# Kernel optimization log

Hardware: AMD Instinct MI355X
Metric: run time of the kernel (lower is better)

## Reference

```python
import jax, jax.numpy as jnp
import numpy as np

H, DH = 16, 64  # n_head, head_dim


def setup_inputs() -> dict:
    key = jax.random.key(0)
    ks = jax.random.split(key, 14)
    B, L, D = 2, 1024, 1024
    d = DH

    def lin_w(k, fan_in, shape):
        return jax.random.normal(k, shape, jnp.float32) / np.sqrt(fan_in)

    return {
        "x": jax.random.normal(ks[0], (B, L, D), jnp.float32),
        "Wq": lin_w(ks[1], D, (D, D)),
        "bq": jnp.zeros((D,), jnp.float32),
        "Wk1": lin_w(ks[2], D, (D, D)),
        "bk1": jnp.zeros((D,), jnp.float32),
        "Wk2": lin_w(ks[3], D, (D, D)),
        "bk2": jnp.zeros((D,), jnp.float32),
        "Wg": lin_w(ks[4], d, (d, 1)),
        "bg": jnp.zeros((1,), jnp.float32),
        "Ws": lin_w(ks[5], d, (d, 1)),
        "bs": jnp.zeros((1,), jnp.float32),
        "Wp": lin_w(ks[6], D, (D, D)),
        "bp": jnp.zeros((D,), jnp.float32),
    }


def reference(x, Wq, bq, Wk1, bk1, Wk2, bk2, Wg, bg, Ws, bs, Wp, bp):
    B, L, D = x.shape
    d = DH
    # AR (GLA) branch
    Q = (x @ Wq + bq).reshape(B, L, H, d)
    K = (x @ Wk1 + bk1).reshape(B, L, H, d)
    V = x.reshape(B, L, H, d)
    W = jnp.einsum('blhd,blhe->blhde', K, V)  # (B,L,H,d,d) outer products
    # stable cumprod of sigmoid gate via log-cumsum-exp trick
    G = jax.nn.sigmoid(x.reshape(B, L, H, d) @ Wg + bg)            # (B,L,H,1)
    log_cum = jnp.clip(jnp.cumsum(jnp.log(jnp.clip(G, 1e-6, None)), axis=1), -30.0, 30.0)
    Gc = (jnp.exp(log_cum) + 1e-6)[..., None]                       # (B,L,H,1,1)
    R = jax.nn.silu(K @ Ws + bs)[..., None]                         # (B,L,H,1,1) decay gate
    Wc = jnp.cumsum(W * R / Gc, axis=1) * Gc                        # weighted cumsum
    O1 = jnp.einsum('blhd,blhde->blhe', Q, Wc)                      # (B,L,H,d)
    # MA branch on one-step residuals
    E = V[:, 1:] - O1[:, :-1]                                       # (B,L-1,H,d)
    q2 = -jax.nn.leaky_relu(-Q[:, :-1] / np.sqrt(d), 0.02)          # ma_q_activation (scale head_dim)
    k2 = jax.nn.sigmoid((x[:, :-1] @ Wk2 + bk2) / np.sqrt(D) * 0.02)  # ma_k_activation (scale n_embd)
    k2 = k2.reshape(B, L - 1, H, d)
    W_ma = jnp.cumsum(jnp.einsum('blhd,blhe->blhde', k2, E), axis=1)
    O2 = jnp.einsum('blhd,blhde->blhe', q2, W_ma)
    O2 = jnp.concatenate([jnp.zeros_like(O2[:, :1]), O2], axis=1)   # shift: first MA output is 0
    O = (O1 + O2).reshape(B, L, D)
    return O @ Wp + bp
```

## Files before the change

kernel.cpp:

```cpp
#include <hip/hip_runtime.h>
#include <hip/hip_bf16.h>
#include <math.h>

#define B_  2
#define L_  1024
#define D_  1024
#define H_  16
#define DH_ 64
#define M_  (B_*L_)
#define CHUNK 64
#define NCH (L_/CHUNK)
#define PT 72
#define PS 68

#define KSCALE (0.02f/32.0f)

using bf16x8 = __attribute__((ext_vector_type(8))) short;
using f32x4  = __attribute__((ext_vector_type(4))) float;

__device__ __forceinline__ unsigned short bf16r(float f){
  union{float f; unsigned int u;} x; x.f = f;
  unsigned int r = x.u + 0x7FFF + ((x.u>>16)&1);
  return (unsigned short)(r>>16);
}
__device__ __forceinline__ float bf2f(unsigned short u){
  union{unsigned int u; float f;} x; x.u = ((unsigned int)u)<<16; return x.f;
}

__device__ __forceinline__ void gate_prefix(
  const float* __restrict__ GL, const float* __restrict__ RR,
  int bh, int c, int l, float* cf_s, float* gc_s)
{
  const float* g = GL + (size_t)bh*L_;
  float part = 0.f;
  for (int i = l; i < c*64; i += 64) part += g[i];
  #pragma unroll
  for (int off = 32; off; off >>= 1) part += __shfl_xor(part, off);
  float x = g[c*64 + l];
  #pragma unroll
  for (int off = 1; off < 64; off <<= 1){
    float t = __shfl_up(x, off);
    if (l >= off) x += t;
  }
  float cum = part + x;
  float lc = fminf(fmaxf(cum, -30.f), 30.f);
  float gc = expf(lc) + 1e-6f;
  cf_s[l] = RR[(size_t)bh*L_ + c*64 + l] / gc;
  if (gc_s) gc_s[l] = gc;
}

__device__ __forceinline__ void chunk_carry(
  const float* __restrict__ csb, int c, int tid, float* carry)
{
  #pragma unroll
  for (int i=0;i<16;i++) carry[i] = 0.f;
  const float4* cb = (const float4*)(csb + (size_t)tid*16);
  #pragma unroll 2
  for (int c2=0;c2<c;c2++){
    const float4* p4 = cb + (size_t)c2*1024;
    float4 a0=p4[0],a1=p4[1],a2=p4[2],a3=p4[3];
    carry[0]+=a0.x; carry[1]+=a0.y; carry[2]+=a0.z; carry[3]+=a0.w;
    carry[4]+=a1.x; carry[5]+=a1.y; carry[6]+=a1.z; carry[7]+=a1.w;
    carry[8]+=a2.x; carry[9]+=a2.y; carry[10]+=a2.z; carry[11]+=a2.w;
    carry[12]+=a3.x; carry[13]+=a3.y; carry[14]+=a3.z; carry[15]+=a3.w;
  }
}

__global__ __launch_bounds__(256) void convert_all(
  const float* __restrict__ X,
  const float* __restrict__ W0, const float* __restrict__ W1,
  const float* __restrict__ W2, const float* __restrict__ W3,
  unsigned short* __restrict__ Xbf,
  unsigned short* __restrict__ T0, unsigned short* __restrict__ T1,
  unsigned short* __restrict__ T2, unsigned short* __restrict__ T3)
{
  int z = blockIdx.z;
  if (z == 4) {
    int row = blockIdx.x*64 + (threadIdx.x>>2);
    int col = blockIdx.y*64 + (threadIdx.x&3)*16;
    const float4* src = (const float4*)&X[(size_t)row*D_ + col];
    float4 a=src[0], b=src[1], c=src[2], d=src[3];
    unsigned short buf[16] = {
      bf16r(a.x),bf16r(a.y),bf16r(a.z),bf16r(a.w),
      bf16r(b.x),bf16r(b.y),bf16r(b.z),bf16r(b.w),
      bf16r(c.x),bf16r(c.y),bf16r(c.z),bf16r(c.w),
      bf16r(d.x),bf16r(d.y),bf16r(d.z),bf16r(d.w)};
    *(uint4*)&Xbf[(size_t)row*D_ + col]     = *(uint4*)&buf[0];
    *(uint4*)&Xbf[(size_t)row*D_ + col + 8] = *(uint4*)&buf[8];
    return;
  }
  if (blockIdx.x >= 16) return;
  const float* W = z==0?W0: z==1?W1: z==2?W2: W3;
  unsigned short* T = z==0?T0: z==1?T1: z==2?T2: T3;
  __shared__ float tile[64][65];
  int kBase = blockIdx.x*64, nBase = blockIdx.y*64;
  #pragma unroll
  for (int i=0;i<16;i++){
    int idx = threadIdx.x + i*256;
    int r = idx>>6, c = idx&63;
    tile[r][c] = W[(size_t)(kBase+r)*D_ + nBase+c];
  }
  __syncthreads();
  #pragma unroll
  for (int i=0;i<16;i++){
    int idx = threadIdx.x + i*256;
    int n = idx>>6, k = idx&63;
    T[(size_t)(nBase+n)*D_ + kBase+k] = bf16r(tile[k][n]);
  }
}

__global__ __launch_bounds__(256) void gemm3(
  const unsigned short* __restrict__ A,
  const unsigned short* __restrict__ T0, const unsigned short* __restrict__ T1,
  const unsigned short* __restrict__ T2,
  const float* __restrict__ b0, const float* __restrict__ b1, const float* __restrict__ b2,
  unsigned short* __restrict__ F0, unsigned short* __restrict__ F1,
  unsigned short* __restrict__ F2)
{
  int z = blockIdx.z;
  const unsigned short* Bt = z==0?T0: z==1?T1: T2;
  const float* bias = z==0?b0: z==1?b1: b2;
  unsigned short* F = z==0?F0: z==1?F1: F2;
  int epi = (z==2) ? 1 : 0;
  int rowBase = blockIdx.x*128, colBase = blockIdx.y*128;

  __shared__ __align__(16) unsigned short As[128*32];
  __shared__ __align__(16) unsigned short Bs[128*32];
  int tid = threadIdx.x, w = tid>>6, l = tid&63;
  int lr = l&15, g4 = l>>4;
  int wr = w>>1, wc = w&1;
  f32x4 acc[4][4];
  #pragma unroll
  for (int mi=0;mi<4;mi++)
    #pragma unroll
    for (int ni=0;ni<4;ni++)
      acc[mi][ni] = (f32x4){0.f,0.f,0.f,0.f};

  for (int k0 = 0; k0 < D_; k0 += 32) {
    #pragma unroll
    for (int i=0;i<2;i++){
      int Fi = (w*2+i)*64 + l;
      int r = Fi>>2, c16 = Fi&3;
      int sc = c16 ^ ((r>>1)&3);
      const unsigned short* ga = A  + (size_t)(rowBase+r)*D_ + k0 + sc*8;
      const unsigned short* gb = Bt + (size_t)(colBase+r)*D_ + k0 + sc*8;
      __builtin_amdgcn_global_load_lds(
        (const __attribute__((address_space(1))) void*)ga,
        (__attribute__((address_space(3))) void*)(As + (size_t)(w*2+i)*512), 16, 0, 0);
      __builtin_amdgcn_global_load_lds(
        (const __attribute__((address_space(1))) void*)gb,
        (__attribute__((address_space(3))) void*)(Bs + (size_t)(w*2+i)*512), 16, 0, 0);
    }
    __syncthreads();
    bf16x8 af[4], bfr[4];
    #pragma unroll
    for (int mi=0;mi<4;mi++){
      int row = wr*64 + mi*16 + lr;
      af[mi] = *(const bf16x8*)(As + row*32 + ((g4 ^ ((row>>1)&3))*8));
    }
    #pragma unroll
    for (int ni=0;ni<4;ni++){
      int n = wc*64 + ni*16 + lr;
      bfr[ni] = *(const bf16x8*)(Bs + n*32 + ((g4 ^ ((n>>1)&3))*8));
    }
    #pragma unroll
    for (int mi=0;mi<4;mi++)
      #pragma unroll
      for (int ni=0;ni<4;ni++)
        acc[mi][ni] = __builtin_amdgcn_mfma_f32_16x16x32_bf16(af[mi], bfr[ni], acc[mi][ni], 0,0,0);
    __syncthreads();
  }

  #pragma unroll
  for (int mi=0;mi<4;mi++){
    #pragma unroll
    for (int ni=0;ni<4;ni++){
      int col = colBase + wc*64 + ni*16 + lr;
      float bv = bias[col];
      #pragma unroll
      for (int r=0;r<4;r++){
        int row = rowBase + wr*64 + mi*16 + g4*4 + r;
        float v = acc[mi][ni][r] + bv;
        if (epi) v = 1.f/(1.f + expf(-v*KSCALE));
        F[(size_t)row*D_ + col] = bf16r(v);
      }
    }
  }
}

__global__ __launch_bounds__(256) void gemm1(
  const unsigned short* __restrict__ A, const unsigned short* __restrict__ Bt,
  const float* __restrict__ bias, float* __restrict__ C)
{
  int rowBase = blockIdx.x*128, colBase = blockIdx.y*64;
  __shared__ __align__(16) unsigned short As[128*32];
  __shared__ __align__(16) unsigned short Bs[64*32];
  int tid = threadIdx.x, w = tid>>6, l = tid&63;
  int lr = l&15, g4 = l>>4;
  f32x4 acc[2][4];
  #pragma unroll
  for (int mi=0;mi<2;mi++)
    #pragma unroll
    for (int ni=0;ni<4;ni++)
      acc[mi][ni] = (f32x4){0.f,0.f,0.f,0.f};

  for (int k0 = 0; k0 < D_; k0 += 32) {
    #pragma unroll
    for (int i=0;i<2;i++){
      int F = (w*2+i)*64 + l;
      int r = F>>2, c16 = F&3;
      int sc = c16 ^ ((r>>1)&3);
      const unsigned short* g = A + (size_t)(rowBase+r)*D_ + k0 + sc*8;
      __builtin_amdgcn_global_load_lds(
        (const __attribute__((address_space(1))) void*)g,
        (__attribute__((address_space(3))) void*)(As + (size_t)(w*2+i)*512), 16, 0, 0);
    }
    {
      int F = w*64 + l;
      int r = F>>2, c16 = F&3;
      int sc = c16 ^ ((r>>1)&3);
      const unsigned short* g = Bt + (size_t)(colBase+r)*D_ + k0 + sc*8;
      __builtin_amdgcn_global_load_lds(
        (const __attribute__((address_space(1))) void*)g,
        (__attribute__((address_space(3))) void*)(Bs + (size_t)w*512), 16, 0, 0);
    }
    __syncthreads();
    bf16x8 af[2], bfr[4];
    #pragma unroll
    for (int mi=0;mi<2;mi++){
      int row = w*32 + mi*16 + lr;
      af[mi] = *(const bf16x8*)(As + row*32 + ((g4 ^ ((row>>1)&3))*8));
    }
    #pragma unroll
    for (int ni=0;ni<4;ni++){
      int n = ni*16 + lr;
      bfr[ni] = *(const bf16x8*)(Bs + n*32 + ((g4 ^ ((n>>1)&3))*8));
    }
    #pragma unroll
    for (int mi=0;mi<2;mi++)
      #pragma unroll
      for (int ni=0;ni<4;ni++)
        acc[mi][ni] = __builtin_amdgcn_mfma_f32_16x16x32_bf16(af[mi], bfr[ni], acc[mi][ni], 0,0,0);
    __syncthreads();
  }

  #pragma unroll
  for (int mi=0;mi<2;mi++){
    #pragma unroll
    for (int ni=0;ni<4;ni++){
      int col = colBase + ni*16 + lr;
      float bv = bias[col];
      #pragma unroll
      for (int r=0;r<4;r++){
        int row = rowBase + w*32 + mi*16 + g4*4 + r;
        C[(size_t)row*D_ + col] = acc[mi][ni][r] + bv;
      }
    }
  }
}

__global__ __launch_bounds__(256) void scalars_kernel(
  const float* __restrict__ X, const unsigned short* __restrict__ Kbf,
  const float* __restrict__ Wg, const float* __restrict__ bg,
  const float* __restrict__ Ws, const float* __restrict__ bs,
  float* __restrict__ GL, float* __restrict__ RR)
{
  int item = blockIdx.x * 4 + (threadIdx.x >> 6);
  int ln = threadIdx.x & 63;
  int row = item >> 4;
  int h = item & 15;
  float xv = X[(size_t)row*D_ + h*64 + ln];
  float kv = bf2f(Kbf[(size_t)row*D_ + h*64 + ln]);
  float gdot = xv * Wg[ln];
  float rdot = kv * Ws[ln];
  #pragma unroll
  for (int off = 32; off; off >>= 1) {
    gdot += __shfl_xor(gdot, off);
    rdot += __shfl_xor(rdot, off);
  }
  if (ln == 0) {
    int b = row >> 10, l = row & 1023;
    size_t o = (size_t)(b*16 + h)*L_ + l;
    float glogit = gdot + bg[0];
    float sg = 1.f/(1.f+expf(-glogit));
    sg = fmaxf(sg, 1e-6f);
    GL[o] = logf(sg);
    float rlogit = rdot + bs[0];
    RR[o] = rlogit / (1.f + expf(-rlogit));
  }
}

__global__ __launch_bounds__(256) void ar_chunk_sum(
  const unsigned short* __restrict__ Kbf, const unsigned short* __restrict__ Xbf,
  const float* __restrict__ GL, const float* __restrict__ RR,
  float* __restrict__ CS)
{
  int bh = blockIdx.x, c = blockIdx.y;
  int b = bh >> 4, h = bh & 15;
  int row0 = b*L_ + c*CHUNK;
  __shared__ __align__(16) unsigned short kt_t[64*PT];
  __shared__ __align__(16) unsigned short cv_t[64*PT];
  __shared__ __align__(16) float uni[64*PS];
  __shared__ float cf_s[64];
  int tid = threadIdx.x;
  if (tid < 64) gate_prefix(GL, RR, bh, c, tid, cf_s, nullptr);
  __syncthreads();
  const unsigned short* kg = Kbf + (size_t)row0*D_ + h*64;
  const unsigned short* vg = Xbf + (size_t)row0*D_ + h*64;
  #pragma unroll
  for (int t=0;t<2;t++){
    int j = (tid>>3) + t*32;
    int d0 = (tid&7)*8;
    bf16x8 kv = *(const bf16x8*)&kg[(size_t)j*D_ + d0];
    bf16x8 vv = *(const bf16x8*)&vg[(size_t)j*D_ + d0];
    float cfj = cf_s[j];
    #pragma unroll
    for (int i=0;i<8;i++){
      kt_t[(d0+i)*PT + j] = (unsigned short)kv[i];
      cv_t[(d0+i)*PT + j] = bf16r(bf2f((unsigned short)vv[i]) * cfj);
    }
  }
  __syncthreads();
  int w = tid>>6, l = tid&63, lr = l&15, g4 = l>>4;
  f32x4 acc[4];
  #pragma unroll
  for (int ni=0;ni<4;ni++) acc[ni] = (f32x4){0.f,0.f,0.f,0.f};
  #pragma unroll
  for (int kk=0;kk<2;kk++){
    bf16x8 a = *(const bf16x8*)&cv_t[(w*16+lr)*PT + kk*32 + g4*8];
    #pragma unroll
    for (int ni=0;ni<4;ni++){
      bf16x8 bb = *(const bf16x8*)&kt_t[(ni*16+lr)*PT + kk*32 + g4*8];
      acc[ni] = __builtin_amdgcn_mfma_f32_16x16x32_bf16(a, bb, acc[ni], 0,0,0);
    }
  }
  #pragma unroll
  for (int ni=0;ni<4;ni++)
    #pragma unroll
    for (int r=0;r<4;r++)
      uni[(w*16+g4*4+r)*PS + ni*16+lr] = acc[ni][r];
  __syncthreads();
  float* out = CS + ((size_t)bh*NCH + c)*4096;
  #pragma unroll
  for (int t=0;t<4;t++){
    int idx = tid + t*256;
    int r = idx>>4, s = idx&15;
    *(float4*)&out[r*64 + s*4] = *(float4*)&uni[r*PS + s*4];
  }
}

__global__ __launch_bounds__(256) void ar_o1_fused(
  const unsigned short* __restrict__ Qbf, const unsigned short* __restrict__ Kbf,
  const unsigned short* __restrict__ Xbf, const unsigned short* __restrict__ K2bf,
  const float* __restrict__ GL, const float* __restrict__ RR,
  const float* __restrict__ CSA, float* __restrict__ CSM,
  float* __restrict__ O1)
{
  int bh = blockIdx.x, c = blockIdx.y;
  int b = bh >> 4, h = bh & 15;
  int row0 = b*L_ + c*CHUNK;
  __shared__ __align__(16) unsigned short q_t[64*PT];
  __shared__ __align__(16) unsigned short k_t[64*PT];
  __shared__ __align__(16) unsigned short vt_t[64*PT];
  __shared__ __align__(16) float uni[64*PS];
  unsigned short* p_t = (unsigned short*)uni;
  __shared__ float cf_s[64], gc_s[64];
  int tid = threadIdx.x;
  if (tid < 64) gate_prefix(GL, RR, bh, c, tid, cf_s, gc_s);
  const unsigned short* qg = Qbf + (size_t)row0*D_ + h*64;
  const unsigned short* kg = Kbf + (size_t)row0*D_ + h*64;
  const unsigned short* vg = Xbf + (size_t)row0*D_ + h*64;
  float carry[16];
  chunk_carry(CSA + (size_t)bh*NCH*4096, c, tid, carry);
  #pragma unroll
  for (int t=0;t<2;t++){
    int idx = tid + t*256;
    int j = idx>>3, s = idx&7;
    *(uint4*)&q_t[j*PT + s*8] = *(const uint4*)&qg[(size_t)j*D_ + s*8];
    *(uint4*)&k_t[j*PT + s*8] = *(const uint4*)&kg[(size_t)j*D_ + s*8];
  }
  #pragma unroll
  for (int t=0;t<2;t++){
    int j = (tid>>3) + t*32;
    int e0 = (tid&7)*8;
    bf16x8 vv = *(const bf16x8*)&vg[(size_t)j*D_ + e0];
    #pragma unroll
    for (int i=0;i<8;i++) vt_t[(e0+i)*PT + j] = (unsigned short)vv[i];
  }
  __syncthreads();
  int w = tid>>6, l = tid&63, lr = l&15, g4 = l>>4;
  f32x4 acc[4];
  #pragma unroll
  for (int ni=0;ni<4;ni++) acc[ni] = (f32x4){0.f,0.f,0.f,0.f};
  #pragma unroll
  for (int kk=0;kk<2;kk++){
    bf16x8 a = *(const bf16x8*)&q_t[(w*16+lr)*PT + kk*32 + g4*8];
    #pragma unroll
    for (int ni=0;ni<4;ni++){
      bf16x8 bb = *(const bf16x8*)&k_t[(ni*16+lr)*PT + kk*32 + g4*8];
      acc[ni] = __builtin_amdgcn_mfma_f32_16x16x32_bf16(a, bb, acc[ni], 0,0,0);
    }
  }
  #pragma unroll
  for (int ni=0;ni<4;ni++){
    int j = ni*16 + lr;
    float cf = cf_s[j];
    #pragma unroll
    for (int r=0;r<4;r++){
      int row = w*16 + g4*4 + r;
      float v = (j <= row) ? acc[ni][r]*cf : 0.f;
      p_t[row*PT + j] = bf16r(v);
    }
  }
  __syncthreads();
  {
    unsigned short buf[16];
    #pragma unroll
    for (int i=0;i<16;i++) buf[i] = bf16r(carry[i]);
    int row = tid>>2, col = (tid&3)*16;
    *(uint4*)&k_t[row*PT + col]     = *(uint4*)&buf[0];
    *(uint4*)&k_t[row*PT + col + 8] = *(uint4*)&buf[8];
  }
  __syncthreads();
  #pragma unroll
  for (int ni=0;ni<4;ni++) acc[ni] = (f32x4){0.f,0.f,0.f,0.f};
  #pragma unroll
  for (int kk=0;kk<2;kk++){
    bf16x8 ap = *(const bf16x8*)&p_t[(w*16+lr)*PT + kk*32 + g4*8];
    bf16x8 aq = *(const bf16x8*)&q_t[(w*16+lr)*PT + kk*32 + g4*8];
    #pragma unroll
    for (int ni=0;ni<4;ni++){
      bf16x8 bv = *(const bf16x8*)&vt_t[(ni*16+lr)*PT + kk*32 + g4*8];
      bf16x8 bs = *(const bf16x8*)&k_t[(ni*16+lr)*PT + kk*32 + g4*8];
      acc[ni] = __builtin_amdgcn_mfma_f32_16x16x32_bf16(ap, bv, acc[ni], 0,0,0);
      acc[ni] = __builtin_amdgcn_mfma_f32_16x16x32_bf16(aq, bs, acc[ni], 0,0,0);
    }
  }
  __syncthreads();
  #pragma unroll
  for (int ni=0;ni<4;ni++)
    #pragma unroll
    for (int r=0;r<4;r++){
      int row = w*16 + g4*4 + r;
      uni[row*PS + ni*16 + lr] = gc_s[row]*acc[ni][r];
    }
  __syncthreads();
  #pragma unroll
  for (int t=0;t<4;t++){
    int idx = tid + t*256;
    int r = idx>>4, s = idx&15;
    *(float4*)&O1[(size_t)(row0+r)*D_ + h*64 + s*4] = *(float4*)&uni[r*PS + s*4];
  }
  #pragma unroll
  for (int t=0;t<2;t++){
    int j = (tid>>3) + t*32;
    int d0 = (tid&7)*8;
    bf16x8 kv = *(const bf16x8*)&K2bf[(size_t)(row0+j)*D_ + h*64 + d0];
    float ev[8] = {0.f,0.f,0.f,0.f,0.f,0.f,0.f,0.f};
    if (c*CHUNK + j < L_-1){
      bf16x8 xv = *(const bf16x8*)&Xbf[(size_t)(row0+j+1)*D_ + h*64 + d0];
      #pragma unroll
      for (int i=0;i<8;i++) ev[i] = bf2f((unsigned short)xv[i]) - uni[j*PS + d0 + i];
    }
    #pragma unroll
    for (int i=0;i<8;i++){
      vt_t[(d0+i)*PT + j] = (unsigned short)kv[i];
      k_t [(d0+i)*PT + j] = bf16r(ev[i]);
    }
  }
  __syncthreads();
  f32x4 acc2[4];
  #pragma unroll
  for (int ni=0;ni<4;ni++) acc2[ni] = (f32x4){0.f,0.f,0.f,0.f};
  #pragma unroll
  for (int kk=0;kk<2;kk++){
    bf16x8 a = *(const bf16x8*)&k_t[(w*16+lr)*PT + kk*32 + g4*8];
    #pragma unroll
    for (int ni=0;ni<4;ni++){
      bf16x8 bb = *(const bf16x8*)&vt_t[(ni*16+lr)*PT + kk*32 + g4*8];
      acc2[ni] = __builtin_amdgcn_mfma_f32_16x16x32_bf16(a, bb, acc2[ni], 0,0,0);
    }
  }
  __syncthreads();
  #pragma unroll
  for (int ni=0;ni<4;ni++)
    #pragma unroll
    for (int r=0;r<4;r++)
      uni[(w*16+g4*4+r)*PS + ni*16+lr] = acc2[ni][r];
  __syncthreads();
  float* outm = CSM + ((size_t)bh*NCH + c)*4096;
  #pragma unroll
  for (int t=0;t<4;t++){
    int idx = tid + t*256;
    int r = idx>>4, s = idx&15;
    *(float4*)&outm[r*64 + s*4] = *(float4*)&uni[r*PS + s*4];
  }
}

__global__ __launch_bounds__(256) void ma_o2_mfma(
  const unsigned short* __restrict__ Qbf, const unsigned short* __restrict__ K2bf,
  const unsigned short* __restrict__ Xbf, const float* __restrict__ CS,
  const float* __restrict__ O1, unsigned short* __restrict__ Obf)
{
  int bh = blockIdx.x, c = blockIdx.y;
  int b = bh >> 4, h = bh & 15;
  int row0 = b*L_ + c*CHUNK;
  __shared__ __align__(16) unsigned short q_t[64*PT];
  __shared__ __align__(16) unsigned short k_t[64*PT];
  __shared__ __align__(16) unsigned short et_t[64*PT];
  __shared__ __align__(16) float uni[64*PS];
  unsigned short* p_t = (unsigned short*)uni;
  int tid = threadIdx.x;
  const unsigned short* qg = Qbf  + (size_t)row0*D_ + h*64;
  const unsigned short* kg = K2bf + (size_t)row0*D_ + h*64;
  float carry[16];
  chunk_carry(CS + (size_t)bh*NCH*4096, c, tid, carry);
  #pragma unroll
  for (int t=0;t<2;t++){
    int idx = tid + t*256;
    int j = idx>>3, s = idx&7;
    *(uint4*)&k_t[j*PT + s*8] = *(const uint4*)&kg[(size_t)j*D_ + s*8];
  }
  #pragma unroll
  for (int t=0;t<2;t++){
    int j = (tid>>3) + t*32;
    int d0 = (tid&7)*8;
    bf16x8 qv = *(const bf16x8*)&qg[(size_t)j*D_ + d0];
    unsigned short qb[8];
    #pragma unroll
    for (int i=0;i<8;i++){
      float q = bf2f((unsigned short)qv[i]);
      qb[i] = bf16r((q > 0.f ? 0.02f*q : q) * 0.125f);
    }
    *(uint4*)&q_t[j*PT + d0] = *(uint4*)&qb[0];
    float ev[8] = {0.f,0.f,0.f,0.f,0.f,0.f,0.f,0.f};
    if (c*CHUNK + j < L_-1){
      bf16x8 xv = *(const bf16x8*)&Xbf[(size_t)(row0+j+1)*D_ + h*64 + d0];
      const float4* op = (const float4*)&O1[(size_t)(row0+j)*D_ + h*64 + d0];
      float4 o0 = op[0], o1v = op[1];
      ev[0]=bf2f((unsigned short)xv[0])-o0.x;  ev[1]=bf2f((unsigned short)xv[1])-o0.y;
      ev[2]=bf2f((unsigned short)xv[2])-o0.z;  ev[3]=bf2f((unsigned short)xv[3])-o0.w;
      ev[4]=bf2f((unsigned short)xv[4])-o1v.x; ev[5]=bf2f((unsigned short)xv[5])-o1v.y;
      ev[6]=bf2f((unsigned short)xv[6])-o1v.z; ev[7]=bf2f((unsigned short)xv[7])-o1v.w;
    }
    #pragma unroll
    for (int i=0;i<8;i++) et_t[(d0+i)*PT + j] = bf16r(ev[i]);
  }
  __syncthreads();
  int w = tid>>6, l = tid&63, lr = l&15, g4 = l>>4;
  f32x4 acc[4];
  #pragma unroll
  for (int ni=0;ni<4;ni++) acc[ni] = (f32x4){0.f,0.f,0.f,0.f};
  #pragma unroll
  for (int kk=0;kk<2;kk++){
    bf16x8 a = *(const bf16x8*)&q_t[(w*16+lr)*PT + kk*32 + g4*8];
    #pragma unroll
    for (int ni=0;ni<4;ni++){
      bf16x8 bb = *(const bf16x8*)&k_t[(ni*16+lr)*PT + kk*32 + g4*8];
      acc[ni] = __builtin_amdgcn_mfma_f32_16x16x32_bf16(a, bb, acc[ni], 0,0,0);
    }
  }
  #pragma unroll
  for (int ni=0;ni<4;ni++){
    int j = ni*16 + lr;
    #pragma unroll
    for (int r=0;r<4;r++){
      int row = w*16 + g4*4 + r;
      float v = (j <= row) ? acc[ni][r] : 0.f;
      p_t[row*PT + j] = bf16r(v);
    }
  }
  __syncthreads();
  {
    unsigned short buf[16];
    #pragma unroll
    for (int i=0;i<16;i++) buf[i] = bf16r(carry[i]);
    int row = tid>>2, col = (tid&3)*16;
    *(uint4*)&k_t[row*PT + col]     = *(uint4*)&buf[0];
    *(uint4*)&k_t[row*PT + col + 8] = *(uint4*)&buf[8];
  }
  __syncthreads();
  #pragma unroll
  for (int ni=0;ni<4;ni++) acc[ni] = (f32x4){0.f,0.f,0.f,0.f};
  #pragma unroll
  for (int kk=0;kk<2;kk++){
    bf16x8 ap = *(const bf16x8*)&p_t[(w*16+lr)*PT + kk*32 + g4*8];
    bf16x8 aq = *(const bf16x8*)&q_t[(w*16+lr)*PT + kk*32 + g4*8];
    #pragma unroll
    for (int ni=0;ni<4;ni++){
      bf16x8 be = *(const bf16x8*)&et_t[(ni*16+lr)*PT + kk*32 + g4*8];
      bf16x8 bt = *(const bf16x8*)&k_t[(ni*16+lr)*PT + kk*32 + g4*8];
      acc[ni] = __builtin_amdgcn_mfma_f32_16x16x32_bf16(ap, be, acc[ni], 0,0,0);
      acc[ni] = __builtin_amdgcn_mfma_f32_16x16x32_bf16(aq, bt, acc[ni], 0,0,0);
    }
  }
  __syncthreads();
  #pragma unroll
  for (int ni=0;ni<4;ni++)
    #pragma unroll
    for (int r=0;r<4;r++){
      int row = w*16 + g4*4 + r;
      uni[row*PS + ni*16 + lr] = acc[ni][r];
    }
  __syncthreads();
  #pragma unroll
  for (int t=0;t<4;t++){
    int idx = tid + t*256;
    int r = idx>>4, s = idx&15;
    if (c*CHUNK + r < L_-1) {
      const float4 gv = *(const float4*)&O1[(size_t)(row0+r+1)*D_ + h*64 + s*4];
      float4 uv = *(float4*)&uni[r*PS + s*4];
      ushort4 o;
      o.x = bf16r(gv.x+uv.x); o.y = bf16r(gv.y+uv.y);
      o.z = bf16r(gv.z+uv.z); o.w = bf16r(gv.w+uv.w);
      *(ushort4*)&Obf[(size_t)(row0+r+1)*D_ + h*64 + s*4] = o;
    }
  }
  if (c == 0 && tid < 16) {
    const float4 gv = *(const float4*)&O1[(size_t)row0*D_ + h*64 + tid*4];
    ushort4 o;
    o.x = bf16r(gv.x); o.y = bf16r(gv.y); o.z = bf16r(gv.z); o.w = bf16r(gv.w);
    *(ushort4*)&Obf[(size_t)row0*D_ + h*64 + tid*4] = o;
  }
}

extern "C" void kernel_launch(void* const* d_in, const int* in_sizes, int n_in,
                              void* d_out, int out_size, void* d_ws, size_t ws_size,
                              hipStream_t stream) {
  const float* x  = (const float*)d_in[0];
  const float* Wq = (const float*)d_in[1];
  const float* bq = (const float*)d_in[2];
  const float* Wk1= (const float*)d_in[3];
  const float* bk1= (const float*)d_in[4];
  const float* Wk2= (const float*)d_in[5];
  const float* bk2= (const float*)d_in[6];
  const float* Wg = (const float*)d_in[7];
  const float* bg = (const float*)d_in[8];
  const float* Ws = (const float*)d_in[9];
  const float* bs = (const float*)d_in[10];
  const float* Wp = (const float*)d_in[11];
  const float* bp = (const float*)d_in[12];
  float* out = (float*)d_out;

  float* ws = (float*)d_ws;
  size_t MD = (size_t)M_*D_;
  float* O1b = ws;
  float* CSA = O1b + MD;
  float* CSM = CSA + (size_t)32*NCH*4096;
  float* GLb = CSM + (size_t)32*NCH*4096;
  float* RRb = GLb + (size_t)32*L_;
  unsigned short* Xbf   = (unsigned short*)(RRb + (size_t)32*L_);
  unsigned short* Qbfs  = Xbf  + MD;
  unsigned short* Kbfs  = Qbfs + MD;
  unsigned short* K2bfs = Kbfs + MD;
  unsigned short* Obf   = K2bfs+ MD;
  unsigned short* Wt0   = Obf + MD;
  unsigned short* Wt1   = Wt0 + (size_t)D_*D_;
  unsigned short* Wt2   = Wt1 + (size_t)D_*D_;
  unsigned short* Wt3   = Wt2 + (size_t)D_*D_;

  dim3 gcv(32, 16, 5);
  convert_all<<<gcv, 256, 0, stream>>>(x, Wq, Wk1, Wk2, Wp, Xbf, Wt0, Wt1, Wt2, Wt3);

  dim3 gg(M_/128, D_/128, 3);
  gemm3<<<gg, 256, 0, stream>>>(Xbf, Wt0, Wt1, Wt2, bq, bk1, bk2, Qbfs, Kbfs, K2bfs);

  scalars_kernel<<<(M_*H_)/4, 256, 0, stream>>>(x, Kbfs, Wg, bg, Ws, bs, GLb, RRb);

  dim3 gc(32, NCH);
  ar_chunk_sum<<<gc, 256, 0, stream>>>(Kbfs, Xbf, GLb, RRb, CSA);
  ar_o1_fused<<<gc, 256, 0, stream>>>(Qbfs, Kbfs, Xbf, K2bfs, GLb, RRb, CSA, CSM, O1b);
  ma_o2_mfma<<<gc, 256, 0, stream>>>(Qbfs, K2bfs, Xbf, CSM, O1b, Obf);

  dim3 go(M_/128, D_/64);
  gemm1<<<go, 256, 0, stream>>>(Obf, Wt3, bp, out);
}
```

Before: 180.2 us.

## Fuse gate scalars into convert/GEMM epilogues, widen GEMM K-tile, swizzle transposed LDS

Drops the separate scalars kernel. The sigmoid-gate log is now computed while converting x to bf16, and the silu decay gate is computed from fp32 K in the K-projection GEMM epilogue through a cross-lane reduction. Both GEMMs move from a K tile of 32 to 64 with an 8-way XOR swizzle, which halves the number of barrier-separated iterations at the cost of more LDS per block. The transposed LDS stores in the chunk kernels gain an XOR column swizzle to cut bank conflicts, and one LDS read is vectorised to float4.

After: 168.5 us. -6.5%, faster.

```diff
diff --git a/kernel.cpp b/kernel.cpp
--- a/kernel.cpp
+++ b/kernel.cpp
@@ -70,14 +70,18 @@
   const float* __restrict__ X,
   const float* __restrict__ W0, const float* __restrict__ W1,
   const float* __restrict__ W2, const float* __restrict__ W3,
+  const float* __restrict__ Wg, const float* __restrict__ bg,
   unsigned short* __restrict__ Xbf,
   unsigned short* __restrict__ T0, unsigned short* __restrict__ T1,
-  unsigned short* __restrict__ T2, unsigned short* __restrict__ T3)
+  unsigned short* __restrict__ T2, unsigned short* __restrict__ T3,
+  float* __restrict__ GL)
 {
   int z = blockIdx.z;
   if (z == 4) {
-    int row = blockIdx.x*64 + (threadIdx.x>>2);
-    int col = blockIdx.y*64 + (threadIdx.x&3)*16;
+    int r4 = threadIdx.x>>2, cq = threadIdx.x&3;
+    int row = blockIdx.x*64 + r4;
+    int h = blockIdx.y;
+    int col = h*64 + cq*16;
     const float4* src = (const float4*)&X[(size_t)row*D_ + col];
     float4 a=src[0], b=src[1], c=src[2], d=src[3];
     unsigned short buf[16] = {
@@ -87,6 +91,20 @@
       bf16r(d.x),bf16r(d.y),bf16r(d.z),bf16r(d.w)};
     *(uint4*)&Xbf[(size_t)row*D_ + col]     = *(uint4*)&buf[0];
     *(uint4*)&Xbf[(size_t)row*D_ + col + 8] = *(uint4*)&buf[8];
+    const float4* wg = (const float4*)&Wg[cq*16];
+    float4 w0=wg[0],w1=wg[1],w2=wg[2],w3=wg[3];
+    float gd = a.x*w0.x+a.y*w0.y+a.z*w0.z+a.w*w0.w
+             + b.x*w1.x+b.y*w1.y+b.z*w1.z+b.w*w1.w
+             + c.x*w2.x+c.y*w2.y+c.z*w2.z+c.w*w2.w
+             + d.x*w3.x+d.y*w3.y+d.z*w3.z+d.w*w3.w;
+    gd += __shfl_xor(gd,1); gd += __shfl_xor(gd,2);
+    if (cq == 0){
+      int bb = row>>10, ll = row&1023;
+      float glogit = gd + bg[0];
+      float sg = 1.f/(1.f+expf(-glogit));
+      sg = fmaxf(sg, 1e-6f);
+      GL[(size_t)(bb*16+h)*L_ + ll] = logf(sg);
+    }
     return;
   }
   if (blockIdx.x >= 16) return;
@@ -114,8 +132,9 @@
   const unsigned short* __restrict__ T0, const unsigned short* __restrict__ T1,
   const unsigned short* __restrict__ T2,
   const float* __restrict__ b0, const float* __restrict__ b1, const float* __restrict__ b2,
+  const float* __restrict__ Ws, const float* __restrict__ bs,
   unsigned short* __restrict__ F0, unsigned short* __restrict__ F1,
-  unsigned short* __restrict__ F2)
+  unsigned short* __restrict__ F2, float* __restrict__ RR)
 {
   int z = blockIdx.z;
   const unsigned short* Bt = z==0?T0: z==1?T1: T2;
@@ -124,8 +143,8 @@
   int epi = (z==2) ? 1 : 0;
   int rowBase = blockIdx.x*128, colBase = blockIdx.y*128;
 
-  __shared__ __align__(16) unsigned short As[128*32];
-  __shared__ __align__(16) unsigned short Bs[128*32];
+  __shared__ __align__(16) unsigned short As[128*64];
+  __shared__ __align__(16) unsigned short Bs[128*64];
   int tid = threadIdx.x, w = tid>>6, l = tid&63;
   int lr = l&15, g4 = l>>4;
   int wr = w>>1, wc = w&1;
@@ -136,41 +155,50 @@
     for (int ni=0;ni<4;ni++)
       acc[mi][ni] = (f32x4){0.f,0.f,0.f,0.f};
 
-  for (int k0 = 0; k0 < D_; k0 += 32) {
-    #pragma unroll
-    for (int i=0;i<2;i++){
-      int Fi = (w*2+i)*64 + l;
-      int r = Fi>>2, c16 = Fi&3;
-      int sc = c16 ^ ((r>>1)&3);
+  for (int k0 = 0; k0 < D_; k0 += 64) {
+    #pragma unroll
+    for (int i=0;i<4;i++){
+      int Fi = (w*4+i)*64 + l;
+      int r = Fi>>3, cc = Fi&7;
+      int sc = cc ^ (r&7);
       const unsigned short* ga = A  + (size_t)(rowBase+r)*D_ + k0 + sc*8;
       const unsigned short* gb = Bt + (size_t)(colBase+r)*D_ + k0 + sc*8;
       __builtin_amdgcn_global_load_lds(
         (const __attribute__((address_space(1))) void*)ga,
-        (__attribute__((address_space(3))) void*)(As + (size_t)(w*2+i)*512), 16, 0, 0);
+        (__attribute__((address_space(3))) void*)(As + (size_t)(w*4+i)*512), 16, 0, 0);
       __builtin_amdgcn_global_load_lds(
         (const __attribute__((address_space(1))) void*)gb,
-        (__attribute__((address_space(3))) void*)(Bs + (size_t)(w*2+i)*512), 16, 0, 0);
+        (__attribute__((address_space(3))) void*)(Bs + (size_t)(w*4+i)*512), 16, 0, 0);
     }
     __syncthreads();
-    bf16x8 af[4], bfr[4];
-    #pragma unroll
-    for (int mi=0;mi<4;mi++){
-      int row = wr*64 + mi*16 + lr;
-      af[mi] = *(const bf16x8*)(As + row*32 + ((g4 ^ ((row>>1)&3))*8));
-    }
-    #pragma unroll
-    for (int ni=0;ni<4;ni++){
-      int n = wc*64 + ni*16 + lr;
-      bfr[ni] = *(const bf16x8*)(Bs + n*32 + ((g4 ^ ((n>>1)&3))*8));
-    }
-    #pragma unroll
-    for (int mi=0;mi<4;mi++)
-      #pragma unroll
-      for (int ni=0;ni<4;ni++)
-        acc[mi][ni] = __builtin_amdgcn_mfma_f32_16x16x32_bf16(af[mi], bfr[ni], acc[mi][ni], 0,0,0);
+    #pragma unroll
+    for (int kk=0;kk<2;kk++){
+      bf16x8 af[4], bfr[4];
+      #pragma unroll
+      for (int mi=0;mi<4;mi++){
+        int row = wr*64 + mi*16 + lr;
+        af[mi] = *(const bf16x8*)(As + row*64 + (((kk*4+g4) ^ (lr&7))<<3));
+      }
+      #pragma unroll
+      for (int ni=0;ni<4;ni++){
+        int n = wc*64 + ni*16 + lr;
+        bfr[ni] = *(const bf16x8*)(Bs + n*64 + (((kk*4+g4) ^ (lr&7))<<3));
+      }
+      #pragma unroll
+      for (int mi=0;mi<4;mi++)
+        #pragma unroll
+        for (int ni=0;ni<4;ni++)
+          acc[mi][ni] = __builtin_amdgcn_mfma_f32_16x16x32_bf16(af[mi], bfr[ni], acc[mi][ni], 0,0,0);
+    }
     __syncthreads();
   }
 
+  float wsv[4];
+  if (z==1){
+    #pragma unroll
+    for (int ni=0;ni<4;ni++) wsv[ni] = Ws[ni*16 + lr];
+  }
+  float rr[4][4] = {};
   #pragma unroll
   for (int mi=0;mi<4;mi++){
     #pragma unroll
@@ -181,10 +209,28 @@
       for (int r=0;r<4;r++){
         int row = rowBase + wr*64 + mi*16 + g4*4 + r;
         float v = acc[mi][ni][r] + bv;
+        if (z==1) rr[mi][r] += v * wsv[ni];
         if (epi) v = 1.f/(1.f + expf(-v*KSCALE));
         F[(size_t)row*D_ + col] = bf16r(v);
       }
     }
+  }
+  if (z==1){
+    int h = (colBase>>6) + wc;
+    #pragma unroll
+    for (int mi=0;mi<4;mi++)
+      #pragma unroll
+      for (int r=0;r<4;r++){
+        float t = rr[mi][r];
+        t += __shfl_xor(t,1); t += __shfl_xor(t,2);
+        t += __shfl_xor(t,4); t += __shfl_xor(t,8);
+        if (lr == 0){
+          int row = rowBase + wr*64 + mi*16 + g4*4 + r;
+          int bb = row>>10, ll = row&1023;
+          float rl = t + bs[0];
+          RR[(size_t)(bb*16+h)*L_ + ll] = rl/(1.f+expf(-rl));
+        }
+      }
   }
 }
 
@@ -193,8 +239,8 @@
   const float* __restrict__ bias, float* __restrict__ C)
 {
   int rowBase = blockIdx.x*128, colBase = blockIdx.y*64;
-  __shared__ __align__(16) unsigned short As[128*32];
-  __shared__ __align__(16) unsigned short Bs[64*32];
+  __shared__ __align__(16) unsigned short As[128*64];
+  __shared__ __align__(16) unsigned short Bs[64*64];
   int tid = threadIdx.x, w = tid>>6, l = tid&63;
   int lr = l&15, g4 = l>>4;
   f32x4 acc[2][4];
@@ -204,43 +250,47 @@
     for (int ni=0;ni<4;ni++)
       acc[mi][ni] = (f32x4){0.f,0.f,0.f,0.f};
 
-  for (int k0 = 0; k0 < D_; k0 += 32) {
-    #pragma unroll
-    for (int i=0;i<2;i++){
-      int F = (w*2+i)*64 + l;
-      int r = F>>2, c16 = F&3;
-      int sc = c16 ^ ((r>>1)&3);
+  for (int k0 = 0; k0 < D_; k0 += 64) {
+    #pragma unroll
+    for (int i=0;i<4;i++){
+      int Fi = (w*4+i)*64 + l;
+      int r = Fi>>3, cc = Fi&7;
+      int sc = cc ^ (r&7);
       const unsigned short* g = A + (size_t)(rowBase+r)*D_ + k0 + sc*8;
       __builtin_amdgcn_global_load_lds(
         (const __attribute__((address_space(1))) void*)g,
-        (__attribute__((address_space(3))) void*)(As + (size_t)(w*2+i)*512), 16, 0, 0);
-    }
-    {
-      int F = w*64 + l;
-      int r = F>>2, c16 = F&3;
-      int sc = c16 ^ ((r>>1)&3);
+        (__attribute__((address_space(3))) void*)(As + (size_t)(w*4+i)*512), 16, 0, 0);
+    }
+    #pragma unroll
+    for (int i=0;i<2;i++){
+      int Fi = (w*2+i)*64 + l;
+      int r = Fi>>3, cc = Fi&7;
+      int sc = cc ^ (r&7);
       const unsigned short* g = Bt + (size_t)(colBase+r)*D_ + k0 + sc*8;
       __builtin_amdgcn_global_load_lds(
         (const __attribute__((address_space(1))) void*)g,
-        (__attribute__((address_space(3))) void*)(Bs + (size_t)w*512), 16, 0, 0);
+        (__attribute__((address_space(3))) void*)(Bs + (size_t)(w*2+i)*512), 16, 0, 0);
     }
     __syncthreads();
-    bf16x8 af[2], bfr[4];
-    #pragma unroll
-    for (int mi=0;mi<2;mi++){
-      int row = w*32 + mi*16 + lr;
-      af[mi] = *(const bf16x8*)(As + row*32 + ((g4 ^ ((row>>1)&3))*8));
-    }
-    #pragma unroll
-    for (int ni=0;ni<4;ni++){
-      int n = ni*16 + lr;
-      bfr[ni] = *(const bf16x8*)(Bs + n*32 + ((g4 ^ ((n>>1)&3))*8));
-    }
-    #pragma unroll
-    for (int mi=0;mi<2;mi++)
-      #pragma unroll
-      for (int ni=0;ni<4;ni++)
-        acc[mi][ni] = __builtin_amdgcn_mfma_f32_16x16x32_bf16(af[mi], bfr[ni], acc[mi][ni], 0,0,0);
+    #pragma unroll
+    for (int kk=0;kk<2;kk++){
+      bf16x8 af[2], bfr[4];
+      #pragma unroll
+      for (int mi=0;mi<2;mi++){
+        int row = w*32 + mi*16 + lr;
+        af[mi] = *(const bf16x8*)(As + row*64 + (((kk*4+g4) ^ (lr&7))<<3));
+      }
+      #pragma unroll
+      for (int ni=0;ni<4;ni++){
+        int n = ni*16 + lr;
+        bfr[ni] = *(const bf16x8*)(Bs + n*64 + (((kk*4+g4) ^ (lr&7))<<3));
+      }
+      #pragma unroll
+      for (int mi=0;mi<2;mi++)
+        #pragma unroll
+        for (int ni=0;ni<4;ni++)
+          acc[mi][ni] = __builtin_amdgcn_mfma_f32_16x16x32_bf16(af[mi], bfr[ni], acc[mi][ni], 0,0,0);
+    }
     __syncthreads();
   }
 
@@ -256,37 +306,6 @@
         C[(size_t)row*D_ + col] = acc[mi][ni][r] + bv;
       }
     }
-  }
-}
-
-__global__ __launch_bounds__(256) void scalars_kernel(
-  const float* __restrict__ X, const unsigned short* __restrict__ Kbf,
-  const float* __restrict__ Wg, const float* __restrict__ bg,
-  const float* __restrict__ Ws, const float* __restrict__ bs,
-  float* __restrict__ GL, float* __restrict__ RR)
-{
-  int item = blockIdx.x * 4 + (threadIdx.x >> 6);
-  int ln = threadIdx.x & 63;
-  int row = item >> 4;
-  int h = item & 15;
-  float xv = X[(size_t)row*D_ + h*64 + ln];
-  float kv = bf2f(Kbf[(size_t)row*D_ + h*64 + ln]);
-  float gdot = xv * Wg[ln];
-  float rdot = kv * Ws[ln];
-  #pragma unroll
-  for (int off = 32; off; off >>= 1) {
-    gdot += __shfl_xor(gdot, off);
-    rdot += __shfl_xor(rdot, off);
-  }
-  if (ln == 0) {
-    int b = row >> 10, l = row & 1023;
-    size_t o = (size_t)(b*16 + h)*L_ + l;
-    float glogit = gdot + bg[0];
-    float sg = 1.f/(1.f+expf(-glogit));
-    sg = fmaxf(sg, 1e-6f);
-    GL[o] = logf(sg);
-    float rlogit = rdot + bs[0];
-    RR[o] = rlogit / (1.f + expf(-rlogit));
   }
 }
 
@@ -311,26 +330,29 @@
   for (int t=0;t<2;t++){
     int j = (tid>>3) + t*32;
     int d0 = (tid&7)*8;
+    int col = (((j>>3) ^ (tid&7))<<3) + (j&7);
     bf16x8 kv = *(const bf16x8*)&kg[(size_t)j*D_ + d0];
     bf16x8 vv = *(const bf16x8*)&vg[(size_t)j*D_ + d0];
     float cfj = cf_s[j];
     #pragma unroll
     for (int i=0;i<8;i++){
-      kt_t[(d0+i)*PT + j] = (unsigned short)kv[i];
-      cv_t[(d0+i)*PT + j] = bf16r(bf2f((unsigned short)vv[i]) * cfj);
+      kt_t[(d0+i)*PT + col] = (unsigned short)kv[i];
+      cv_t[(d0+i)*PT + col] = bf16r(bf2f((unsigned short)vv[i]) * cfj);
     }
   }
   __syncthreads();
   int w = tid>>6, l = tid&63, lr = l&15, g4 = l>>4;
+  int ha = (w*2 + (lr>>3)) & 7;
   f32x4 acc[4];
   #pragma unroll
   for (int ni=0;ni<4;ni++) acc[ni] = (f32x4){0.f,0.f,0.f,0.f};
   #pragma unroll
   for (int kk=0;kk<2;kk++){
-    bf16x8 a = *(const bf16x8*)&cv_t[(w*16+lr)*PT + kk*32 + g4*8];
+    bf16x8 a = *(const bf16x8*)&cv_t[(w*16+lr)*PT + (((kk*4+g4) ^ ha)<<3)];
     #pragma unroll
     for (int ni=0;ni<4;ni++){
-      bf16x8 bb = *(const bf16x8*)&kt_t[(ni*16+lr)*PT + kk*32 + g4*8];
+      int hb = (ni*2 + (lr>>3)) & 7;
+      bf16x8 bb = *(const bf16x8*)&kt_t[(ni*16+lr)*PT + (((kk*4+g4) ^ hb)<<3)];
       acc[ni] = __builtin_amdgcn_mfma_f32_16x16x32_bf16(a, bb, acc[ni], 0,0,0);
     }
   }
@@ -383,12 +405,14 @@
   for (int t=0;t<2;t++){
     int j = (tid>>3) + t*32;
     int e0 = (tid&7)*8;
+    int col = (((j>>3) ^ (tid&7))<<3) + (j&7);
     bf16x8 vv = *(const bf16x8*)&vg[(size_t)j*D_ + e0];
     #pragma unroll
-    for (int i=0;i<8;i++) vt_t[(e0+i)*PT + j] = (unsigned short)vv[i];
+    for (int i=0;i<8;i++) vt_t[(e0+i)*PT + col] = (unsigned short)vv[i];
   }
   __syncthreads();
   int w = tid>>6, l = tid&63, lr = l&15, g4 = l>>4;
+  int ha = (w*2 + (lr>>3)) & 7;
   f32x4 acc[4];
   #pragma unroll
   for (int ni=0;ni<4;ni++) acc[ni] = (f32x4){0.f,0.f,0.f,0.f};
@@ -430,7 +454,8 @@
     bf16x8 aq = *(const bf16x8*)&q_t[(w*16+lr)*PT + kk*32 + g4*8];
     #pragma unroll
     for (int ni=0;ni<4;ni++){
-      bf16x8 bv = *(const bf16x8*)&vt_t[(ni*16+lr)*PT + kk*32 + g4*8];
+      int hb = (ni*2 + (lr>>3)) & 7;
+      bf16x8 bv = *(const bf16x8*)&vt_t[(ni*16+lr)*PT + (((kk*4+g4) ^ hb)<<3)];
       bf16x8 bs = *(const bf16x8*)&k_t[(ni*16+lr)*PT + kk*32 + g4*8];
       acc[ni] = __builtin_amdgcn_mfma_f32_16x16x32_bf16(ap, bv, acc[ni], 0,0,0);
       acc[ni] = __builtin_amdgcn_mfma_f32_16x16x32_bf16(aq, bs, acc[ni], 0,0,0);
@@ -455,17 +480,22 @@
   for (int t=0;t<2;t++){
     int j = (tid>>3) + t*32;
     int d0 = (tid&7)*8;
+    int col = (((j>>3) ^ (tid&7))<<3) + (j&7);
     bf16x8 kv = *(const bf16x8*)&K2bf[(size_t)(row0+j)*D_ + h*64 + d0];
     float ev[8] = {0.f,0.f,0.f,0.f,0.f,0.f,0.f,0.f};
     if (c*CHUNK + j < L_-1){
       bf16x8 xv = *(const bf16x8*)&Xbf[(size_t)(row0+j+1)*D_ + h*64 + d0];
-      #pragma unroll
-      for (int i=0;i<8;i++) ev[i] = bf2f((unsigned short)xv[i]) - uni[j*PS + d0 + i];
+      const float4* up = (const float4*)&uni[j*PS + d0];
+      float4 u0 = up[0], u1 = up[1];
+      ev[0]=bf2f((unsigned short)xv[0])-u0.x; ev[1]=bf2f((unsigned short)xv[1])-u0.y;
+      ev[2]=bf2f((unsigned short)xv[2])-u0.z; ev[3]=bf2f((unsigned short)xv[3])-u0.w;
+      ev[4]=bf2f((unsigned short)xv[4])-u1.x; ev[5]=bf2f((unsigned short)xv[5])-u1.y;
+      ev[6]=bf2f((unsigned short)xv[6])-u1.z; ev[7]=bf2f((unsigned short)xv[7])-u1.w;
     }
     #pragma unroll
     for (int i=0;i<8;i++){
-      vt_t[(d0+i)*PT + j] = (unsigned short)kv[i];
-      k_t [(d0+i)*PT + j] = bf16r(ev[i]);
+      vt_t[(d0+i)*PT + col] = (unsigned short)kv[i];
+      k_t [(d0+i)*PT + col] = bf16r(ev[i]);
     }
   }
   __syncthreads();
@@ -474,10 +504,11 @@
   for (int ni=0;ni<4;ni++) acc2[ni] = (f32x4){0.f,0.f,0.f,0.f};
   #pragma unroll
   for (int kk=0;kk<2;kk++){
-    bf16x8 a = *(const bf16x8*)&k_t[(w*16+lr)*PT + kk*32 + g4*8];
+    bf16x8 a = *(const bf16x8*)&k_t[(w*16+lr)*PT + (((kk*4+g4) ^ ha)<<3)];
     #pragma unroll
     for (int ni=0;ni<4;ni++){
-      bf16x8 bb = *(const bf16x8*)&vt_t[(ni*16+lr)*PT + kk*32 + g4*8];
+      int hb = (ni*2 + (lr>>3)) & 7;
+      bf16x8 bb = *(const bf16x8*)&vt_t[(ni*16+lr)*PT + (((kk*4+g4) ^ hb)<<3)];
       acc2[ni] = __builtin_amdgcn_mfma_f32_16x16x32_bf16(a, bb, acc2[ni], 0,0,0);
     }
   }
@@ -525,6 +556,7 @@
   for (int t=0;t<2;t++){
     int j = (tid>>3) + t*32;
     int d0 = (tid&7)*8;
+    int col = (((j>>3) ^ (tid&7))<<3) + (j&7);
     bf16x8 qv = *(const bf16x8*)&qg[(size_t)j*D_ + d0];
     unsigned short qb[8];
     #pragma unroll
@@ -544,7 +576,7 @@
       ev[6]=bf2f((unsigned short)xv[6])-o1v.z; ev[7]=bf2f((unsigned short)xv[7])-o1v.w;
     }
     #pragma unroll
-    for (int i=0;i<8;i++) et_t[(d0+i)*PT + j] = bf16r(ev[i]);
+    for (int i=0;i<8;i++) et_t[(d0+i)*PT + col] = bf16r(ev[i]);
   }
   __syncthreads();
   int w = tid>>6, l = tid&63, lr = l&15, g4 = l>>4;
@@ -588,7 +620,8 @@
     bf16x8 aq = *(const bf16x8*)&q_t[(w*16+lr)*PT + kk*32 + g4*8];
     #pragma unroll
     for (int ni=0;ni<4;ni++){
-      bf16x8 be = *(const bf16x8*)&et_t[(ni*16+lr)*PT + kk*32 + g4*8];
+      int hb = (ni*2 + (lr>>3)) & 7;
+      bf16x8 be = *(const bf16x8*)&et_t[(ni*16+lr)*PT + (((kk*4+g4) ^ hb)<<3)];
       bf16x8 bt = *(const bf16x8*)&k_t[(ni*16+lr)*PT + kk*32 + g4*8];
       acc[ni] = __builtin_amdgcn_mfma_f32_16x16x32_bf16(ap, be, acc[ni], 0,0,0);
       acc[ni] = __builtin_amdgcn_mfma_f32_16x16x32_bf16(aq, bt, acc[ni], 0,0,0);
@@ -660,12 +693,12 @@
   unsigned short* Wt3   = Wt2 + (size_t)D_*D_;
 
   dim3 gcv(32, 16, 5);
-  convert_all<<<gcv, 256, 0, stream>>>(x, Wq, Wk1, Wk2, Wp, Xbf, Wt0, Wt1, Wt2, Wt3);
+  convert_all<<<gcv, 256, 0, stream>>>(x, Wq, Wk1, Wk2, Wp, Wg, bg,
+                                       Xbf, Wt0, Wt1, Wt2, Wt3, GLb);
 
   dim3 gg(M_/128, D_/128, 3);
-  gemm3<<<gg, 256, 0, stream>>>(Xbf, Wt0, Wt1, Wt2, bq, bk1, bk2, Qbfs, Kbfs, K2bfs);
-
-  scalars_kernel<<<(M_*H_)/4, 256, 0, stream>>>(x, Kbfs, Wg, bg, Ws, bs, GLb, RRb);
+  gemm3<<<gg, 256, 0, stream>>>(Xbf, Wt0, Wt1, Wt2, bq, bk1, bk2, Ws, bs,
+                                Qbfs, Kbfs, K2bfs, RRb);
 
   dim3 gc(32, NCH);
   ar_chunk_sum<<<gc, 256, 0, stream>>>(Kbfs, Xbf, GLb, RRb, CSA);
```
